# Optimization experiments

Measured on AMD Instinct MI355X. Metric: run time of the kernel, lower is better.

The kernel has to match this reference:

```python
import jax, jax.numpy as jnp
import numpy as np
from jax import lax

BEAM = 4
MAXLEN = 12
V, E, H = 32000, 256, 512
S, B = 512, 8


def lstm_cell(x, h, c, Wih, Whh, bih, bhh):
    # torch gate order: input, forget, cell, output
    g = x @ Wih.T + h @ Whh.T + bih + bhh
    i, f, gg, o = jnp.split(g, 4, axis=-1)
    c2 = jax.nn.sigmoid(f) * c + jax.nn.sigmoid(i) * jnp.tanh(gg)
    return jax.nn.sigmoid(o) * jnp.tanh(c2), c2


def lstm_layer(xs, Wih, Whh, bih, bhh):
    Bn, Hn = xs.shape[1], Whh.shape[1]
    h0 = jnp.zeros((Bn, Hn), xs.dtype)

    def step(carry, x):
        h, c = carry
        h, c = lstm_cell(x, h, c, Wih, Whh, bih, bhh)
        return (h, c), h

    (hT, cT), hs = lax.scan(step, (h0, h0), xs)
    return hs, hT, cT


def setup_inputs():
    key = jax.random.key(0)
    ks = jax.random.split(key, 32)

    def p(i, shape, s=0.08):
        return jax.random.normal(ks[i], shape, jnp.float32) * s

    return {
        'text': jax.random.randint(ks[0], (S, B), 0, V),
        'emb_enc': p(1, (V, E)),
        'emb_dec': p(2, (V, E)),
        'enc_Wih0': p(3, (4 * H, E)), 'enc_Whh0': p(4, (4 * H, H)),
        'enc_bih0': p(5, (4 * H,)), 'enc_bhh0': p(6, (4 * H,)),
        'enc_Wih1': p(7, (4 * H, H)), 'enc_Whh1': p(8, (4 * H, H)),
        'enc_bih1': p(9, (4 * H,)), 'enc_bhh1': p(10, (4 * H,)),
        'dec_Wih': p(11, (4 * H, E)), 'dec_Whh': p(12, (4 * H, H)),
        'dec_bih': p(13, (4 * H,)), 'dec_bhh': p(14, (4 * H,)),
        'Wq': p(15, (H, H)), 'bq': p(16, (H,)),
        'Wk': p(17, (H, H)), 'bk': p(18, (H,)),
        'Wv': p(19, (H, H)), 'bv': p(20, (H,)),
        'Wo': p(21, (H, H)), 'bo': p(22, (H,)),
        'Wout': p(23, (V, H)), 'bout': p(24, (V,)),
    }


def reference(text, emb_enc, emb_dec, enc_Wih0, enc_Whh0, enc_bih0, enc_bhh0,
              enc_Wih1, enc_Whh1, enc_bih1, enc_bhh1,
              dec_Wih, dec_Whh, dec_bih, dec_bhh,
              Wq, bq, Wk, bk, Wv, bv, Wo, bo, Wout, bout):
    # ---- encoder: 2-layer LSTM over source ----
    emb = emb_enc[text]                                   # [S, B, E]
    hs0, h0, c0 = lstm_layer(emb, enc_Wih0, enc_Whh0, enc_bih0, enc_bhh0)
    hs1, h1, c1 = lstm_layer(hs0, enc_Wih1, enc_Whh1, enc_bih1, enc_bhh1)
    enc_hidden = jnp.stack([h0, h1])                      # [L, B, H] final hidden per layer
    k_enc = enc_hidden @ Wk.T + bk                        # precompute encoder K/V projections
    v_enc = enc_hidden @ Wv.T + bv
    scale = 1.0 / jnp.sqrt(jnp.float32(H))

    # ---- beam state: all beams start from last encoder layer state ----
    dec_h = jnp.tile(h1[None], (BEAM, 1, 1))              # [BEAM, B, H]
    dec_c = jnp.tile(c1[None], (BEAM, 1, 1))
    T = MAXLEN + 1
    result = jnp.full((BEAM, T, B), 1, dtype=jnp.int32)   # SOS token = 1
    logits_hist = jnp.zeros((BEAM, T, B, V), jnp.float32).at[:, 0, :, 1].set(1.0)

    def step(carry, t):
        dh, dc, res, lh = carry
        tok = lax.dynamic_slice(res, (0, t, 0), (BEAM, 1, B))[:, 0, :]      # last token [BEAM, B]
        x = emb_dec[tok]                                                    # [BEAM, B, E]
        nh, nc = lstm_cell(x, dh, dc, dec_Wih, dec_Whh, dec_bih, dec_bhh)   # batched over beams
        # single-head attention: query = dec hidden, keys/values = [enc layers ; dec hidden]
        q = nh @ Wq.T + bq
        kd = nh @ Wk.T + bk
        vd = nh @ Wv.T + bv
        keys = jnp.concatenate([jnp.broadcast_to(k_enc[None], (BEAM,) + k_enc.shape), kd[:, None]], axis=1)  # [BEAM, L+1, B, H]
        vals = jnp.concatenate([jnp.broadcast_to(v_enc[None], (BEAM,) + v_enc.shape), vd[:, None]], axis=1)
        scores = jnp.einsum('nbh,nlbh->nbl', q, keys) * scale
        w = jax.nn.softmax(scores, axis=-1)
        ctx = jnp.einsum('nbl,nlbh->nbh', w, vals)
        dec_out = (ctx @ Wo.T + bo) @ Wout.T + bout                          # [BEAM, B, V]
        # per-beam top-k over vocab, then top-k over the BEAM*BEAM candidates
        pv, pt = lax.top_k(dec_out, BEAM)                                    # [BEAM, B, K]
        cand_v = jnp.transpose(pv, (1, 0, 2)).reshape(B, BEAM * BEAM)        # beam-major blocks
        cand_t = jnp.transpose(pt, (1, 0, 2)).reshape(B, BEAM * BEAM)
        _, ti = lax.top_k(cand_v, BEAM)                                      # [B, K]
        old_beam = (ti // BEAM).T                                            # [BEAM, B]
        new_tok = jnp.take_along_axis(cand_t, ti, axis=1).T                  # [BEAM, B]
        # vectorized beam reorder (gather) of state + history
        nh = jnp.take_along_axis(nh, old_beam[:, :, None], axis=0)
        nc = jnp.take_along_axis(nc, old_beam[:, :, None], axis=0)
        res = jnp.take_along_axis(res, old_beam[:, None, :], axis=0)
        lh = jnp.take_along_axis(lh, old_beam[:, None, :, None], axis=0)
        step_log = jnp.take_along_axis(dec_out, old_beam[:, :, None], axis=0)
        res = lax.dynamic_update_slice(res, new_tok[:, None, :].astype(jnp.int32), (0, t + 1, 0))
        lh = lax.dynamic_update_slice(lh, step_log[:, None], (0, t + 1, 0, 0))
        return (nh, nc, res, lh), None

    (dec_h, dec_c, result, logits_hist), _ = lax.scan(
        step, (dec_h, dec_c, result, logits_hist), jnp.arange(MAXLEN))
    output_res = result[0].T                               # [B, T]
    output_logits = jnp.transpose(logits_hist[0], (1, 2, 0))  # [B, V, T]
    return output_res, output_logits
```

## Files before the change

### kernel.cpp

```cpp
#include <hip/hip_runtime.h>
#include <hip/hip_bf16.h>
#include <float.h>


using ull = unsigned long long;

#define SCOPE_AGENT __HIP_MEMORY_SCOPE_AGENT

__device__ __forceinline__ float cLoad(const float* p) {
  return __hip_atomic_load(p, __ATOMIC_RELAXED, SCOPE_AGENT);
}
__device__ __forceinline__ void cStore(float* p, float v) {
  __hip_atomic_store(p, v, __ATOMIC_RELAXED, SCOPE_AGENT);
}
__device__ __forceinline__ int cLoadI(const int* p) {
  return __hip_atomic_load(p, __ATOMIC_RELAXED, SCOPE_AGENT);
}
__device__ __forceinline__ void cStoreI(int* p, int v) {
  __hip_atomic_store(p, v, __ATOMIC_RELAXED, SCOPE_AGENT);
}
__device__ __forceinline__ ull cLoad64(const ull* p) {
  return __hip_atomic_load(p, __ATOMIC_RELAXED, SCOPE_AGENT);
}
__device__ __forceinline__ void cStore64(ull* p, ull v) {
  __hip_atomic_store(p, v, __ATOMIC_RELAXED, SCOPE_AGENT);
}

__device__ __forceinline__ float2 u2f2(ull u) {
  union { ull u; float2 f; } c; c.u = u; return c.f;
}

__device__ __forceinline__ bool isSent(ull v) {
  return (unsigned)v == 0xFFFFFFFFu || (unsigned)(v >> 32) == 0xFFFFFFFFu;
}

__device__ __forceinline__ void fbar1(int* fl, int phase) {
  __syncthreads();
  if (threadIdx.x < 32)
    cStoreI(fl + (blockIdx.x * 32 + threadIdx.x) * 32, phase);
  {
    const int* f = fl + (threadIdx.x * 32 + (blockIdx.x >> 3)) * 32;
    while (cLoadI(f) < phase) {}
  }
  __syncthreads();
}

__device__ __forceinline__ float sig_(float x) { return 1.0f / (1.0f + expf(-x)); }

__device__ __forceinline__ void ins4(float* v, int* id, float nv, int ni) {
  if (nv > v[3] || (nv == v[3] && ni < id[3])) {
    v[3] = nv; id[3] = ni;
#pragma unroll
    for (int p = 3; p > 0; --p) {
      bool sw = (v[p] > v[p - 1]) || (v[p] == v[p - 1] && id[p] < id[p - 1]);
      if (sw) {
        float t0 = v[p]; v[p] = v[p - 1]; v[p - 1] = t0;
        int t1 = id[p]; id[p] = id[p - 1]; id[p - 1] = t1;
      }
    }
  }
}

struct EncP {
  const int* text; const float* emb;
  const float* Wih0; const float* Whh0; const float* bih0; const float* bhh0;
  const float* Wih1; const float* Whh1; const float* bih1; const float* bhh1;
  float* h0hist; float* h1hist;
  float* h0f; float* h1f; float* c1f;
};

template <int KX>
__device__ void enc_run(const EncP& P, float* xcat, int w, int tid) {
  constexpr int KTOT = KX + 512;
  constexpr int ST = KTOT + 4;
  constexpr int KSL = KTOT / 8;
  constexpr int Q = KSL / 4;
  constexpr int L = (KX == 512) ? 1 : 0;
  __shared__ float part[16 * 8 * 8];
  __shared__ float gl[128];

  const int c0 = (w & 127) * 4;
  const int kh = tid >> 5, col = (tid >> 3) & 3, b = tid & 7;
  const int kbase = kh * KSL;

  const float* Wih = L ? P.Wih1 : P.Wih0;
  const float* Whh = L ? P.Whh1 : P.Whh0;
  const float4* wih4[4]; const float4* whh4[4];
#pragma unroll
  for (int g = 0; g < 4; ++g) {
    const int row = g * 512 + c0 + col;
    wih4[g] = (const float4*)(Wih + (size_t)row * KX);
    whh4[g] = (const float4*)(Whh + (size_t)row * 512);
  }
  float bsum = 0.f;
  if (tid < 128) {
    const int r = tid >> 3;
    const int row = (r & 3) * 512 + c0 + (r >> 2);
    bsum = (L ? P.bih1[row] + P.bhh1[row] : P.bih0[row] + P.bhh0[row]);
  }
  float creg = 0.f;
  float* myHist = L ? P.h1hist : P.h0hist;

  int qx = (KX - kbase) / 4;
  qx = qx < 0 ? 0 : (qx > Q ? Q : qx);

  for (int e = tid; e < 4096; e += 256)
    xcat[(e >> 9) * ST + KX + (e & 511)] = 0.f;
  __syncthreads();

  for (int t = 0; t < 512; ++t) {
    if constexpr (KX == 256) {
      for (int e = tid; e < 1024; e += 256) {
        const int b2 = e >> 7, k2 = e & 127;
        const int tokv = P.text[t * 8 + b2];
        *(float2*)(xcat + b2 * ST + 2 * k2) =
            *(const float2*)(P.emb + (size_t)tokv * 256 + 2 * k2);
      }
      if (t >= 1) {
        const ull* hq = (const ull*)(myHist + (size_t)t * 4096) + tid;
        ull v[8];
#pragma unroll
        for (int z = 0; z < 8; ++z) v[z] = cLoad64(hq + z * 256);
        for (;;) {
          bool any = false;
#pragma unroll
          for (int z = 0; z < 8; ++z)
            if (isSent(v[z])) { v[z] = cLoad64(hq + z * 256); any = true; }
          if (!any) break;
        }
#pragma unroll
        for (int z = 0; z < 8; ++z)
          *(ull*)(xcat + z * ST + KX + 2 * tid) = v[z];
      }
    } else {
      const ull* xq0 = (const ull*)(P.h0hist + (size_t)(t + 1) * 4096) + tid;
      const ull* hq = (const ull*)(P.h1hist + (size_t)t * 4096) + tid;
      ull vx[8], vh[8];
#pragma unroll
      for (int z = 0; z < 8; ++z) vx[z] = cLoad64(xq0 + z * 256);
      if (t >= 1) {
#pragma unroll
        for (int z = 0; z < 8; ++z) vh[z] = cLoad64(hq + z * 256);
      }
      for (;;) {
        bool any = false;
#pragma unroll
        for (int z = 0; z < 8; ++z)
          if (isSent(vx[z])) { vx[z] = cLoad64(xq0 + z * 256); any = true; }
        if (t >= 1) {
#pragma unroll
          for (int z = 0; z < 8; ++z)
            if (isSent(vh[z])) { vh[z] = cLoad64(hq + z * 256); any = true; }
        }
        if (!any) break;
      }
#pragma unroll
      for (int z = 0; z < 8; ++z)
        *(ull*)(xcat + z * ST + 2 * tid) = vx[z];
      if (t >= 1) {
#pragma unroll
        for (int z = 0; z < 8; ++z)
          *(ull*)(xcat + z * ST + KX + 2 * tid) = vh[z];
      }
    }
    __syncthreads();

    float a0 = 0.f, a1 = 0.f, a2 = 0.f, a3 = 0.f;
    {
      const float4* xq = (const float4*)(xcat + b * ST + kbase);
      const int iw = kbase >> 2, ih = (kbase - KX) >> 2;
#pragma unroll 4
      for (int q = 0; q < qx; ++q) {
        float4 x = xq[q];
        float4 w0 = wih4[0][iw + q], w1 = wih4[1][iw + q];
        float4 w2 = wih4[2][iw + q], w3 = wih4[3][iw + q];
        a0 = fmaf(w0.x, x.x, a0); a0 = fmaf(w0.y, x.y, a0);
        a0 = fmaf(w0.z, x.z, a0); a0 = fmaf(w0.w, x.w, a0);
        a1 = fmaf(w1.x, x.x, a1); a1 = fmaf(w1.y, x.y, a1);
        a1 = fmaf(w1.z, x.z, a1); a1 = fmaf(w1.w, x.w, a1);
        a2 = fmaf(w2.x, x.x, a2); a2 = fmaf(w2.y, x.y, a2);
        a2 = fmaf(w2.z, x.z, a2); a2 = fmaf(w2.w, x.w, a2);
        a3 = fmaf(w3.x, x.x, a3); a3 = fmaf(w3.y, x.y, a3);
        a3 = fmaf(w3.z, x.z, a3); a3 = fmaf(w3.w, x.w, a3);
      }
#pragma unroll 4
      for (int q = qx; q < Q; ++q) {
        float4 x = xq[q];
        float4 w0 = whh4[0][ih + q], w1 = whh4[1][ih + q];
        float4 w2 = whh4[2][ih + q], w3 = whh4[3][ih + q];
        a0 = fmaf(w0.x, x.x, a0); a0 = fmaf(w0.y, x.y, a0);
        a0 = fmaf(w0.z, x.z, a0); a0 = fmaf(w0.w, x.w, a0);
        a1 = fmaf(w1.x, x.x, a1); a1 = fmaf(w1.y, x.y, a1);
        a1 = fmaf(w1.z, x.z, a1); a1 = fmaf(w1.w, x.w, a1);
        a2 = fmaf(w2.x, x.x, a2); a2 = fmaf(w2.y, x.y, a2);
        a2 = fmaf(w2.z, x.z, a2); a2 = fmaf(w2.w, x.w, a2);
        a3 = fmaf(w3.x, x.x, a3); a3 = fmaf(w3.y, x.y, a3);
        a3 = fmaf(w3.z, x.z, a3); a3 = fmaf(w3.w, x.w, a3);
      }
    }
    part[((col * 4 + 0) * 8 + b) * 8 + kh] = a0;
    part[((col * 4 + 1) * 8 + b) * 8 + kh] = a1;
    part[((col * 4 + 2) * 8 + b) * 8 + kh] = a2;
    part[((col * 4 + 3) * 8 + b) * 8 + kh] = a3;
    __syncthreads();
    if (tid < 128) {
      const int r = tid >> 3, b2 = tid & 7;
      const float4* pp = (const float4*)(part + (r * 8 + b2) * 8);
      float4 p0 = pp[0], p1 = pp[1];
      gl[r * 8 + b2] =
          bsum + (((p0.x + p0.y) + (p0.z + p0.w)) + ((p1.x + p1.y) + (p1.z + p1.w)));
    }
    __syncthreads();
    if (tid < 32) {
      const int cc = tid >> 3, b2 = tid & 7;
      float gi = gl[(cc * 4 + 0) * 8 + b2], gf_ = gl[(cc * 4 + 1) * 8 + b2];
      float gg = gl[(cc * 4 + 2) * 8 + b2], go = gl[(cc * 4 + 3) * 8 + b2];
      float c2 = sig_(gf_) * creg + sig_(gi) * tanhf(gg);
      float hv = sig_(go) * tanhf(c2);
      creg = c2;
      cStore(myHist + (size_t)(t + 1) * 4096 + b2 * 512 + c0 + cc, hv);
      if (t == 511) {
        (L ? P.h1f : P.h0f)[b2 * 512 + c0 + cc] = hv;
        if (L) P.c1f[b2 * 512 + c0 + cc] = c2;
      }
    }
    __syncthreads();
  }
}

__global__ __launch_bounds__(256, 1) void enc_kernel(EncP P) {
  __shared__ float xcat0[8 * 772];
  __shared__ float xcat1[8 * 1028];
  if (blockIdx.x >> 7) enc_run<512>(P, xcat1, blockIdx.x, threadIdx.x);
  else enc_run<256>(P, xcat0, blockIdx.x, threadIdx.x);
}

__global__ __launch_bounds__(256) void prep_kernel(
    const float* Wk, const float* bk, const float* Wv, const float* bv,
    const float* h0f, const float* h1f, const float* c1f,
    float* kenc, float* venc, float* nhb, float* ncb) {
  const int w = blockIdx.x, tid = threadIdx.x;
  if (w < 64) {
    const int o = w * 256 + tid;
    const int kv = o >> 13, l = (o >> 12) & 1, b = (o >> 9) & 7, c = o & 511;
    const float4* h4 = (const float4*)((l ? h1f : h0f) + b * 512);
    const float4* w4 = (const float4*)((kv ? Wv : Wk) + (size_t)c * 512);
    float s0 = 0.f, s1 = 0.f, s2 = 0.f, s3 = 0.f;
#pragma unroll 8
    for (int k = 0; k < 128; ++k) {
      float4 a = w4[k], x = h4[k];
      s0 = fmaf(a.x, x.x, s0); s1 = fmaf(a.y, x.y, s1);
      s2 = fmaf(a.z, x.z, s2); s3 = fmaf(a.w, x.w, s3);
    }
    (kv ? venc : kenc)[l * 4096 + b * 512 + c] =
        (kv ? bv : bk)[c] + ((s0 + s1) + (s2 + s3));
  } else {
    const int o = (w - 64) * 256 + tid;
    nhb[16384 + o] = h1f[o & 4095];
    ncb[16384 + o] = c1f[o & 4095];
  }
}

__global__ __launch_bounds__(256) void prep2_kernel(
    const float* Wq, const float* Wk, const float* Wv, const float* Wo,
    const float* bq, const float* bk, const float* bv,
    const float* kenc, const float* venc,
    float* At, float* W2, float* u, float* pvec, float* veWo, float* bvo,
    float* sl0, float* sbb) {
  const int w = blockIdx.x, tid = threadIdx.x;
#pragma unroll 1
  for (int sub = 0; sub < 2; ++sub) {
    const int d = 2 * w + sub;
    for (int cc = 0; cc < 2; ++cc) {
      const int c = tid + cc * 256;
      float s0 = 0.f, s1 = 0.f, s2 = 0.f, s3 = 0.f;
      for (int i = 0; i < 512; i += 4) {
        s0 = fmaf(Wk[(i + 0) * 512 + d], Wq[(i + 0) * 512 + c], s0);
        s1 = fmaf(Wk[(i + 1) * 512 + d], Wq[(i + 1) * 512 + c], s1);
        s2 = fmaf(Wk[(i + 2) * 512 + d], Wq[(i + 2) * 512 + c], s2);
        s3 = fmaf(Wk[(i + 3) * 512 + d], Wq[(i + 3) * 512 + c], s3);
      }
      At[(size_t)d * 512 + c] = (s0 + s1) + (s2 + s3);
    }
    for (int cc = 0; cc < 2; ++cc) {
      const int dc = tid + cc * 256;
      float s0 = 0.f, s1 = 0.f, s2 = 0.f, s3 = 0.f;
      const float* wor = Wo + (size_t)d * 512;
      for (int c2 = 0; c2 < 512; c2 += 4) {
        s0 = fmaf(wor[c2 + 0], Wv[(size_t)(c2 + 0) * 512 + dc], s0);
        s1 = fmaf(wor[c2 + 1], Wv[(size_t)(c2 + 1) * 512 + dc], s1);
        s2 = fmaf(wor[c2 + 2], Wv[(size_t)(c2 + 2) * 512 + dc], s2);
        s3 = fmaf(wor[c2 + 3], Wv[(size_t)(c2 + 3) * 512 + dc], s3);
      }
      W2[(size_t)d * 512 + dc] = (s0 + s1) + (s2 + s3);
    }
  }
  if (w == 0) {
    for (int cc = 0; cc < 2; ++cc) {
      const int c = tid + cc * 256;
      float a = 0.f;
      for (int i = 0; i < 512; ++i)
        a += Wq[i * 512 + c] * bk[i] + Wk[i * 512 + c] * bq[i];
      u[c] = a;
    }
  } else if (w <= 32) {
    const int idx = (w - 1) * 256 + tid;
    const int l = idx >> 12, b = (idx >> 9) & 7, c = idx & 511;
    const float* ke = kenc + l * 4096 + b * 512;
    float a = 0.f;
    for (int i = 0; i < 512; ++i) a = fmaf(Wq[i * 512 + c], ke[i], a);
    pvec[idx] = a;
  } else if (w <= 64) {
    const int idx = (w - 33) * 256 + tid;
    const int l = idx >> 12, b = (idx >> 9) & 7, j = idx & 511;
    const float* ve = venc + l * 4096 + b * 512;
    const float* wo = Wo + (size_t)j * 512;
    float a = 0.f;
    for (int c = 0; c < 512; ++c) a = fmaf(wo[c], ve[c], a);
    veWo[idx] = a;
  } else if (w == 65) {
    for (int cc = 0; cc < 2; ++cc) {
      const int j = tid + cc * 256;
      const float* wo = Wo + (size_t)j * 512;
      float a = 0.f;
      for (int c = 0; c < 512; ++c) a = fmaf(wo[c], bv[c], a);
      bvo[j] = a;
    }
  } else if (w == 66) {
    if (tid < 16) {
      const int l = tid >> 3, b = tid & 7;
      const float* ke = kenc + l * 4096 + b * 512;
      float a = 0.f;
      for (int i = 0; i < 512; ++i) a = fmaf(bq[i], ke[i], a);
      sl0[tid] = a;
    } else if (tid == 16) {
      float a = 0.f;
      for (int i = 0; i < 512; ++i) a = fmaf(bq[i], bk[i], a);
      sbb[0] = a;
    }
  }
}

__global__ __launch_bounds__(256) void prep3_kernel(
    const float* Wout, const float* bout, const float* bo, const float* veWo,
    float* E0g, float* E1g, float* bcg) {
  __shared__ float sv[16 * 516 + 512];
  __shared__ float stg[8 * 516];
  const int w = blockIdx.x, tid = threadIdx.x;
  for (int e = tid; e < 8704; e += 256) {
    if (e < 8192) sv[(e >> 9) * 516 + (e & 511)] = veWo[e];
    else sv[16 * 516 + (e - 8192)] = bo[e - 8192];
  }
  const int cbase = w * 125;
  for (int tile = 0; tile < 16; ++tile) {
    const int r0 = tile * 8;
    __syncthreads();
    for (int e = tid; e < 1024; e += 256) {
      const int rr = e >> 7, k4 = e & 127;
      int row = r0 + rr; if (row > 124) row = 124;
      *(float4*)&stg[rr * 516 + k4 * 4] =
          *(const float4*)&Wout[(size_t)(cbase + row) * 512 + k4 * 4];
    }
    __syncthreads();
    if (tid < 136) {
      const int rr = tid / 17, sel = tid - rr * 17;
      const int row = r0 + rr;
      if (row < 125) {
        const float4* a4 = (const float4*)&stg[rr * 516];
        const float4* x4 =
            (const float4*)&sv[sel < 16 ? sel * 516 : 16 * 516];
        float s0 = 0.f, s1 = 0.f, s2 = 0.f, s3 = 0.f;
#pragma unroll 8
        for (int k = 0; k < 128; ++k) {
          float4 a = a4[k], x = x4[k];
          s0 = fmaf(a.x, x.x, s0); s1 = fmaf(a.y, x.y, s1);
          s2 = fmaf(a.z, x.z, s2); s3 = fmaf(a.w, x.w, s3);
        }
        const float s = (s0 + s1) + (s2 + s3);
        const int c = cbase + row;
        if (sel < 16) (sel < 8 ? E0g : E1g)[(size_t)(sel & 7) * 32000 + c] = s;
        else bcg[c] = s + bout[c];
      }
    }
  }
}

struct DecP {
  const float* emb;
  const float* Wih; const float* Whh; const float* bih; const float* bhh;
  const float* Wout;
  const float* At; const float* W2; const float* u; const float* bvo;
  const float* pvec; const float* sl0; const float* sbb;
  const float* E0g; const float* E1g; const float* bcg;
  float* nhb; float* ncb;
  float* vbuf;
  float* part_s;
  ull* pvp;
  int* obh;
  int* res0;
  __hip_bfloat16* hist;
  int* fl;
};

__global__ __launch_bounds__(256, 1) void dec_kernel(DecP P) {
  __shared__ float SM[29600];
  __shared__ float gl[2][4][32];
  __shared__ float slS[32][3];
  __shared__ float wslS[96];
  __shared__ float svv[32][8][4];
  __shared__ int sii[32][8][4];
  __shared__ float rvS[32][4];
  __shared__ int rtS[32][4];
  __shared__ int resS[4][13][8];
  __shared__ int oblS[32];
  __shared__ int tokS[32];
  __shared__ float pscS[32][8];
  __shared__ float nhsS[32][8];

  const int w = blockIdx.x, tid = threadIdx.x;
  float* hs = SM;
  float* tileS = SM;
  float* vqS = SM + 16896;
  float* tvE = SM + 21120;
  int* tiE = (int*)(SM + 25344);
  int ph = 0;

  if (tid < 104) {
    for (int n = 0; n < 4; ++n) resS[n][tid >> 3][tid & 7] = 1;
  }

  auto do_select = [&](int tt) {
    {
      const int r = tid >> 3, ch = tid & 7;
      float m4[4] = {-FLT_MAX, -FLT_MAX, -FLT_MAX, -FLT_MAX};
      int mi[4] = {0x7fffffff, 0x7fffffff, 0x7fffffff, 0x7fffffff};
      for (int g = 0; g < 4; ++g) {
        ull pk[32];
#pragma unroll
        for (int z = 0; z < 32; ++z) {
          const int wg = ch * 32 + g * 8 + (z >> 2);
          pk[z] = cLoad64(P.pvp + wg * 128 + r * 4 + (z & 3));
        }
#pragma unroll
        for (int z = 0; z < 32; ++z)
          ins4(m4, mi, __uint_as_float((unsigned)(pk[z] >> 32)),
               (int)(unsigned)(pk[z] & 0xffffffffu));
      }
#pragma unroll
      for (int k = 0; k < 4; ++k) { svv[r][ch][k] = m4[k]; sii[r][ch][k] = mi[k]; }
    }
    __syncthreads();
    if (tid < 32) {
      float m4[4] = {-FLT_MAX, -FLT_MAX, -FLT_MAX, -FLT_MAX};
      int mi[4] = {0x7fffffff, 0x7fffffff, 0x7fffffff, 0x7fffffff};
      for (int g2 = 0; g2 < 8; ++g2)
#pragma unroll
        for (int k = 0; k < 4; ++k) ins4(m4, mi, svv[tid][g2][k], sii[tid][g2][k]);
#pragma unroll
      for (int k = 0; k < 4; ++k) { rvS[tid][k] = m4[k]; rtS[tid][k] = mi[k]; }
    }
    __syncthreads();
    if (tid < 8) {
      const int b2 = tid;
      unsigned used = 0;
      int obl_[4], tkl_[4];
#pragma unroll
      for (int sel = 0; sel < 4; ++sel) {
        float bestv = -FLT_MAX; int bestj = -1;
        for (int j = 0; j < 16; ++j) {
          if (used & (1u << j)) continue;
          float vv = rvS[(j >> 2) * 8 + b2][j & 3];
          if (vv > bestv) { bestv = vv; bestj = j; }
        }
        used |= 1u << bestj;
        const int obn = bestj >> 2;
        obl_[sel] = obn;
        tkl_[sel] = rtS[obn * 8 + b2][bestj & 3];
        oblS[sel * 8 + b2] = obn;
        tokS[sel * 8 + b2] = tkl_[sel];
        if (w == 0) P.obh[tt * 32 + sel * 8 + b2] = obn;
      }
      if (w == 0) {
        int tmp[4][13];
        for (int n2 = 0; n2 < 4; ++n2)
          for (int s2 = 0; s2 < 13; ++s2) tmp[n2][s2] = resS[obl_[n2]][s2][b2];
        for (int n2 = 0; n2 < 4; ++n2)
          for (int s2 = 0; s2 < 13; ++s2) resS[n2][s2][b2] = tmp[n2][s2];
        for (int n2 = 0; n2 < 4; ++n2) resS[n2][tt + 1][b2] = tkl_[n2];
      }
    }
    __syncthreads();
    if (tt == 11 && w == 0 && tid < 104)
      P.res0[tid] = resS[0][tid >> 3][tid & 7];
  };

  for (int t = 0; t < 12; ++t) {
    const int curOff = (t & 1) * 16384, prevOff = ((t + 1) & 1) * 16384;

    if (t == 0) {
      __syncthreads();
      if (tid < 32) { oblS[tid] = tid >> 3; tokS[tid] = 1; }
      __syncthreads();
    } else {
      do_select(t - 1);
    }
    {
      const int col_l = tid >> 7, gate = (tid >> 5) & 3, nb = tid & 31;
      const int col = 2 * w + col_l;
      const int row = gate * 512 + col;
      for (int e = tid; e < 2048; e += 256) {
        const int nb2 = e >> 6, kf = e & 63;
        float4 v = *((const float4*)(P.emb + (size_t)tokS[nb2] * 256) + kf);
        *((float4*)hs + nb2 * 65 + kf) = v;
      }
      __syncthreads();
      float s0 = 0.f, s1 = 0.f, s2 = 0.f, s3 = 0.f;
      {
        const float4* a4 = (const float4*)(P.Wih + (size_t)row * 256);
        const float4* x4 = (const float4*)hs + nb * 65;
#pragma unroll 8
        for (int k = 0; k < 64; ++k) {
          float4 a = a4[k], x = x4[k];
          s0 = fmaf(a.x, x.x, s0); s1 = fmaf(a.y, x.y, s1);
          s2 = fmaf(a.z, x.z, s2); s3 = fmaf(a.w, x.w, s3);
        }
      }
      float acc = P.bih[row] + P.bhh[row];
      const ull* hsrc = (const ull*)(P.nhb + prevOff);
      const float4* w4row = (const float4*)(P.Whh + (size_t)row * 512);
      for (int ck = 0; ck < 2; ++ck) {
        __syncthreads();
        for (int e = tid; e < 4096; e += 256) {
          const int nb2 = e >> 7, k2 = e & 127;
          const int srow = oblS[nb2] * 8 + (nb2 & 7);
          ull v = cLoad64(hsrc + srow * 256 + ck * 128 + k2);
          *(ull*)(hs + nb2 * 260 + 2 * k2) = v;
        }
        __syncthreads();
        const float4* h4 = (const float4*)hs + nb * 65;
        const float4* w4 = w4row + ck * 64;
#pragma unroll 8
        for (int k = 0; k < 64; ++k) {
          float4 a = w4[k], x = h4[k];
          s0 = fmaf(a.x, x.x, s0); s1 = fmaf(a.y, x.y, s1);
          s2 = fmaf(a.z, x.z, s2); s3 = fmaf(a.w, x.w, s3);
        }
      }
      acc += (s0 + s1) + (s2 + s3);
      gl[col_l][gate][nb] = acc;
      __syncthreads();
      if (tid < 64) {
        const int cc = tid >> 5, nb2 = tid & 31;
        const int col2 = 2 * w + cc;
        float gi = gl[cc][0][nb2], gf_ = gl[cc][1][nb2];
        float gg = gl[cc][2][nb2], go = gl[cc][3][nb2];
        const int srow = oblS[nb2] * 8 + (nb2 & 7);
        float cold = cLoad(P.ncb + prevOff + srow * 512 + col2);
        float c2 = sig_(gf_) * cold + sig_(gi) * tanhf(gg);
        float hv = sig_(go) * tanhf(c2);
        cStore(P.nhb + curOff + nb2 * 512 + col2, hv);
        cStore(P.ncb + curOff + nb2 * 512 + col2, c2);
      }
    }
    fbar1(P.fl, ++ph);

    if (w < 128) {
      const int p = w >> 6, cb = w & 63;
      const int col_l = tid >> 5, nb = tid & 31;
      const int col = cb * 8 + col_l;
      const float* W = (p ? P.W2 : P.At) + (size_t)col * 512;
      float acc = (p ? P.bvo : P.u)[col];
      {
        const float4* w4row = (const float4*)W;
        float s0 = 0.f, s1 = 0.f, s2 = 0.f, s3 = 0.f;
        for (int ck = 0; ck < 2; ++ck) {
          __syncthreads();
          const ull* s8 = (const ull*)(P.nhb + curOff);
          for (int e = tid; e < 4096; e += 256) {
            const int nb2 = e >> 7, k2 = e & 127;
            ull v = cLoad64(s8 + nb2 * 256 + ck * 128 + k2);
            *(ull*)(hs + nb2 * 260 + 2 * k2) = v;
          }
          __syncthreads();
          const float4* h4 = (const float4*)hs + nb * 65;
          const float4* w4 = w4row + ck * 64;
#pragma unroll 8
          for (int k = 0; k < 64; ++k) {
            float4 a = w4[k], x = h4[k];
            s0 = fmaf(a.x, x.x, s0); s1 = fmaf(a.y, x.y, s1);
            s2 = fmaf(a.z, x.z, s2); s3 = fmaf(a.w, x.w, s3);
          }
        }
        acc += (s0 + s1) + (s2 + s3);
      }
      if (p) {
        cStore(P.vbuf + nb * 512 + col, acc);
      } else {
        const float nhv = cLoad(P.nhb + curOff + nb * 512 + col);
        pscS[nb][col_l] = nhv * acc;
        nhsS[nb][col_l] = nhv;
        __syncthreads();
        if (tid < 32) {
          const int nb2 = tid, b = nb2 & 7;
          float s2a = 0.f, l0 = 0.f, l1 = 0.f;
#pragma unroll
          for (int i2 = 0; i2 < 8; ++i2) {
            s2a += pscS[nb2][i2];
            const float nv = nhsS[nb2][i2];
            l0 = fmaf(nv, P.pvec[b * 512 + cb * 8 + i2], l0);
            l1 = fmaf(nv, P.pvec[4096 + b * 512 + cb * 8 + i2], l1);
          }
          cStore(P.part_s + (0 * 32 + nb2) * 64 + cb, l0);
          cStore(P.part_s + (1 * 32 + nb2) * 64 + cb, l1);
          cStore(P.part_s + (2 * 32 + nb2) * 64 + cb, s2a);
        }
      }
    }
    fbar1(P.fl, ++ph);

    {
      const int cbase = w * 125;
      if (tid < 96) {
        const int nb = tid / 3, l = tid - (tid / 3) * 3, b = nb & 7;
        const ull* ps = (const ull*)(P.part_s + (l * 32 + nb) * 64);
        ull pk[32];
#pragma unroll
        for (int z = 0; z < 32; ++z) pk[z] = cLoad64(ps + z);
        float s = 0.f;
#pragma unroll
        for (int z = 0; z < 32; ++z) { float2 f = u2f2(pk[z]); s += f.x + f.y; }
        const float bias = (l < 2) ? P.sl0[l * 8 + b] : P.sbb[0];
        slS[nb][l] = (s + bias) * (1.0f / sqrtf(512.0f));
      }
      __syncthreads();
      if (tid < 32) {
        float a = slS[tid][0], b2 = slS[tid][1], c3 = slS[tid][2];
        float m = fmaxf(a, fmaxf(b2, c3));
        float e0 = expf(a - m), e1 = expf(b2 - m), e2 = expf(c3 - m);
        float inv = 1.0f / (e0 + e1 + e2);
        wslS[tid * 3 + 0] = e0 * inv;
        wslS[tid * 3 + 1] = e1 * inv;
        wslS[tid * 3 + 2] = e2 * inv;
      }
      const int rg = tid >> 3, ng = tid & 7;
      float acc[4][4];
#pragma unroll
      for (int i = 0; i < 4; ++i)
#pragma unroll
        for (int j = 0; j < 4; ++j) acc[i][j] = 0.f;
      for (int q = 0; q < 4; ++q) {
        __syncthreads();
        for (int e = tid; e < 1024; e += 256) {
          const int nb = e >> 5, kf = e & 31;
          ull u0 = cLoad64((const ull*)(P.vbuf + nb * 512 + q * 128 + kf * 4));
          ull u1 = cLoad64((const ull*)(P.vbuf + nb * 512 + q * 128 + kf * 4 + 2));
          float2 a = u2f2(u0), b2 = u2f2(u1);
          float4 v = {a.x, a.y, b2.x, b2.y};
          *(float4*)(vqS + (nb & 3) * 1056 + (nb >> 2) * 132 + kf * 4) = v;
        }
        for (int it = 0; it < 16; ++it) {
          const int idx = it * 256 + tid;
          if (idx < 4000) {
            const int r = idx >> 5, kf = idx & 31;
            float4 v = *(const float4*)(P.Wout + (size_t)(cbase + r) * 512 +
                                        q * 128 + kf * 4);
            *(float4*)(tileS + (r & 3) * 4224 + (r >> 2) * 132 + kf * 4) = v;
          }
        }
        __syncthreads();
        for (int kf = 0; kf < 32; ++kf) {
          float4 xv[4], wv[4];
#pragma unroll
          for (int j = 0; j < 4; ++j)
            xv[j] = *(const float4*)(vqS + j * 1056 + ng * 132 + kf * 4);
#pragma unroll
          for (int i = 0; i < 4; ++i)
            wv[i] = *(const float4*)(tileS + i * 4224 + rg * 132 + kf * 4);
#pragma unroll
          for (int i = 0; i < 4; ++i)
#pragma unroll
            for (int j = 0; j < 4; ++j) {
              float a = acc[i][j];
              a = fmaf(wv[i].x, xv[j].x, a); a = fmaf(wv[i].y, xv[j].y, a);
              a = fmaf(wv[i].z, xv[j].z, a); a = fmaf(wv[i].w, xv[j].w, a);
              acc[i][j] = a;
            }
        }
      }
      __syncthreads();
      float w0w[4], w1w[4], w2w[4];
#pragma unroll
      for (int j = 0; j < 4; ++j) {
        const int nb = ng * 4 + j;
        w0w[j] = wslS[nb * 3 + 0]; w1w[j] = wslS[nb * 3 + 1]; w2w[j] = wslS[nb * 3 + 2];
      }
      float v4[4][4]; int i4[4][4];
#pragma unroll
      for (int j = 0; j < 4; ++j)
#pragma unroll
        for (int k = 0; k < 4; ++k) { v4[j][k] = -FLT_MAX; i4[j][k] = 0x7fffffff; }
#pragma unroll
      for (int i = 0; i < 4; ++i) {
        const int r = rg * 4 + i;
        if (r < 125) {
          const int c = cbase + r;
          const float bcv = P.bcg[c];
#pragma unroll
          for (int j = 0; j < 4; ++j) {
            const int nb = ng * 4 + j, b = nb & 7;
            const float e0 = P.E0g[(size_t)b * 32000 + c];
            const float e1 = P.E1g[(size_t)b * 32000 + c];
            const float L = fmaf(w2w[j], acc[i][j],
                                 fmaf(w0w[j], e0, fmaf(w1w[j], e1, bcv)));
            P.hist[(size_t)t * 1024000 + (size_t)nb * 32000 + c] = __float2bfloat16(L);
            ins4(v4[j], i4[j], L, c);
          }
        }
      }
#pragma unroll
      for (int j = 0; j < 4; ++j)
#pragma unroll
        for (int k = 0; k < 4; ++k) {
          tvE[(ng * 4 + j) * 132 + rg * 4 + k] = v4[j][k];
          tiE[(ng * 4 + j) * 132 + rg * 4 + k] = i4[j][k];
        }
      __syncthreads();
      if (tid < 32) {
        float m4[4] = {-FLT_MAX, -FLT_MAX, -FLT_MAX, -FLT_MAX};
        int mi[4] = {0x7fffffff, 0x7fffffff, 0x7fffffff, 0x7fffffff};
        for (int e = 0; e < 128; ++e)
          ins4(m4, mi, tvE[tid * 132 + e], tiE[tid * 132 + e]);
#pragma unroll
        for (int k = 0; k < 4; ++k) {
          ull pk = ((ull)__float_as_uint(m4[k]) << 32) | (unsigned)mi[k];
          cStore64(P.pvp + w * 128 + tid * 4 + k, pk);
        }
      }
    }
    fbar1(P.fl, ++ph);
  }
  if (w == 0) do_select(11);
}

__global__ __launch_bounds__(256) void out_kernel(const __hip_bfloat16* hist,
                                                  const int* obh, const int* res0,
                                                  float* out) {
  __shared__ float sh[13 * 1000];
  __shared__ int sbArr[12];
  const int w = blockIdx.x, tid = threadIdx.x;
  const int b = w >> 5, v0 = (w & 31) * 1000;
  if (tid == 0) {
    int beta = 0;
    for (int t = 11; t >= 0; --t) {
      const int sb = obh[t * 32 + beta * 8 + b];
      sbArr[t] = sb;
      beta = sb;
    }
  }
  __syncthreads();
  for (int e = tid; e < 12000; e += 256) {
    const int t = e / 1000, vv = e - t * 1000;
    sh[(t + 1) * 1000 + vv] = __bfloat162float(
        hist[(size_t)(t * 32 + sbArr[t] * 8 + b) * 32000 + v0 + vv]);
  }
  for (int e = tid; e < 1000; e += 256) sh[e] = (v0 + e == 1) ? 1.0f : 0.0f;
  __syncthreads();
  float* base = out + 104 + (size_t)(b * 32000 + v0) * 13;
  for (int o = tid; o < 13000; o += 256) {
    const int v = o / 13, t = o - v * 13;
    base[o] = sh[t * 1000 + v];
  }
  if (w == 0 && tid < 104) {
    out[(tid & 7) * 13 + (tid >> 3)] = (float)res0[tid];
  }
}

extern "C" void kernel_launch(void* const* d_in, const int* in_sizes, int n_in,
                              void* d_out, int out_size, void* d_ws, size_t ws_size,
                              hipStream_t stream) {
  const int* text  = (const int*)d_in[0];
  const float* embE = (const float*)d_in[1];
  const float* embD = (const float*)d_in[2];
  const float* Wih0 = (const float*)d_in[3];
  const float* Whh0 = (const float*)d_in[4];
  const float* bih0 = (const float*)d_in[5];
  const float* bhh0 = (const float*)d_in[6];
  const float* Wih1 = (const float*)d_in[7];
  const float* Whh1 = (const float*)d_in[8];
  const float* bih1 = (const float*)d_in[9];
  const float* bhh1 = (const float*)d_in[10];
  const float* dWih = (const float*)d_in[11];
  const float* dWhh = (const float*)d_in[12];
  const float* dbih = (const float*)d_in[13];
  const float* dbhh = (const float*)d_in[14];
  const float* Wq = (const float*)d_in[15];
  const float* bq = (const float*)d_in[16];
  const float* Wk = (const float*)d_in[17];
  const float* bk = (const float*)d_in[18];
  const float* Wv = (const float*)d_in[19];
  const float* bv = (const float*)d_in[20];
  const float* Wo = (const float*)d_in[21];
  const float* bo = (const float*)d_in[22];
  const float* Wout = (const float*)d_in[23];
  const float* bout = (const float*)d_in[24];

  char* ws = (char*)d_ws;
  size_t off = 0;
  auto alloc = [&](size_t bytes) -> char* {
    off = (off + 511) & ~(size_t)511;
    char* p = ws + off;
    off += bytes;
    return p;
  };
  float* h0hist = (float*)alloc((size_t)513 * 4096 * 4);
  float* h1hist = (float*)alloc((size_t)513 * 4096 * 4);
  int* decFl  = (int*)alloc((size_t)262144 * 4);
  float* h0f  = (float*)alloc(4096 * 4);
  float* h1f  = (float*)alloc(4096 * 4);
  float* c1f  = (float*)alloc(4096 * 4);
  float* kenc = (float*)alloc(8192 * 4);
  float* venc = (float*)alloc(8192 * 4);
  float* At   = (float*)alloc((size_t)262144 * 4);
  float* W2   = (float*)alloc((size_t)262144 * 4);
  float* u    = (float*)alloc(512 * 4);
  float* pvec = (float*)alloc(8192 * 4);
  float* veWo = (float*)alloc(8192 * 4);
  float* bvo  = (float*)alloc(512 * 4);
  float* sl0  = (float*)alloc(16 * 4);
  float* sbb  = (float*)alloc(32 * 4);
  float* E0g  = (float*)alloc((size_t)256000 * 4);
  float* E1g  = (float*)alloc((size_t)256000 * 4);
  float* bcg  = (float*)alloc(32000 * 4);
  float* nhb  = (float*)alloc(2 * 16384 * 4);
  float* ncb  = (float*)alloc(2 * 16384 * 4);
  float* vbuf = (float*)alloc(16384 * 4);
  float* part_s = (float*)alloc(6144 * 4);
  ull* pvp    = (ull*)alloc((size_t)32768 * 8);
  int* obh    = (int*)alloc(384 * 4);
  int* res0   = (int*)alloc(104 * 4);
  __hip_bfloat16* hist = (__hip_bfloat16*)alloc((size_t)12288000 * 2);
  if (off > ws_size) return;

  hipMemsetAsync(h0hist, 0xFF, (size_t)513 * 4096 * 4, stream);
  hipMemsetAsync(h1hist, 0xFF, (size_t)513 * 4096 * 4, stream);
  hipMemsetAsync(decFl, 0, (size_t)262144 * 4, stream);

  EncP ep{text, embE, Wih0, Whh0, bih0, bhh0, Wih1, Whh1, bih1, bhh1,
          h0hist, h1hist, h0f, h1f, c1f};
  enc_kernel<<<256, 256, 0, stream>>>(ep);

  prep_kernel<<<128, 256, 0, stream>>>(Wk, bk, Wv, bv, h0f, h1f, c1f, kenc, venc,
                                       nhb, ncb);
  prep2_kernel<<<256, 256, 0, stream>>>(Wq, Wk, Wv, Wo, bq, bk, bv, kenc, venc,
                                        At, W2, u, pvec, veWo, bvo, sl0, sbb);
  prep3_kernel<<<256, 256, 0, stream>>>(Wout, bout, bo, veWo, E0g, E1g, bcg);

  DecP dp{embD, dWih, dWhh, dbih, dbhh, Wout,
          At, W2, u, bvo, pvec, sl0, sbb, E0g, E1g, bcg,
          nhb, ncb, vbuf, part_s, pvp, obh, res0, hist, decFl};
  dec_kernel<<<256, 256, 0, stream>>>(dp);

  out_kernel<<<256, 256, 0, stream>>>(hist, obh, res0, (float*)d_out);
}
```

Measured before the change: 6.337 ms.

## Overlap encoder-independent weight precomputation with the encoder kernel via extra blocks

Work that depends only on the weights (Wk^T·Wq, Wo·Wv, u, bvo, sbb, and the bo-projected output bias) moves out of the post-encoder prep kernels into 256 extra blocks appended to the encoder launch. The recurrent encoder blocks raise their wave priority with s_setprio so the added blocks use idle CUs without slowing the serial LSTM. This shortens the prep kernels that sit on the critical path after the encoder. The risk is that the wing blocks compete with the encoder for memory bandwidth or CU residency. If the encoder's cross-block synchronisation assumes all 256 LSTM blocks are co-resident, the extra blocks could also delay scheduling.

Result: faster. 5.812 ms (-8.3%).

```diff
diff --git a/kernel.cpp b/kernel.cpp
--- a/kernel.cpp
+++ b/kernel.cpp
@@ -67,6 +67,10 @@
   const float* Wih1; const float* Whh1; const float* bih1; const float* bhh1;
   float* h0hist; float* h1hist;
   float* h0f; float* h1f; float* c1f;
+  const float* Wq; const float* Wk; const float* Wv; const float* Wo;
+  const float* bq; const float* bk; const float* bv; const float* bo;
+  const float* Wout; const float* bout;
+  float* At; float* W2; float* u; float* bvo; float* sbb; float* bcg;
 };
 
 template <int KX>
@@ -228,9 +232,80 @@
   }
 }
 
+__device__ void enc_wing(const EncP& P, int wgw, int tid) {
+#pragma unroll 1
+  for (int sub = 0; sub < 2; ++sub) {
+    const int d = 2 * wgw + sub;
+    for (int cc = 0; cc < 2; ++cc) {
+      const int c = tid + cc * 256;
+      float s0 = 0.f, s1 = 0.f, s2 = 0.f, s3 = 0.f;
+      for (int i = 0; i < 512; i += 4) {
+        s0 = fmaf(P.Wk[(i + 0) * 512 + d], P.Wq[(i + 0) * 512 + c], s0);
+        s1 = fmaf(P.Wk[(i + 1) * 512 + d], P.Wq[(i + 1) * 512 + c], s1);
+        s2 = fmaf(P.Wk[(i + 2) * 512 + d], P.Wq[(i + 2) * 512 + c], s2);
+        s3 = fmaf(P.Wk[(i + 3) * 512 + d], P.Wq[(i + 3) * 512 + c], s3);
+      }
+      P.At[(size_t)d * 512 + c] = (s0 + s1) + (s2 + s3);
+    }
+    for (int cc = 0; cc < 2; ++cc) {
+      const int dc = tid + cc * 256;
+      float s0 = 0.f, s1 = 0.f, s2 = 0.f, s3 = 0.f;
+      const float* wor = P.Wo + (size_t)d * 512;
+      for (int c2 = 0; c2 < 512; c2 += 4) {
+        s0 = fmaf(wor[c2 + 0], P.Wv[(size_t)(c2 + 0) * 512 + dc], s0);
+        s1 = fmaf(wor[c2 + 1], P.Wv[(size_t)(c2 + 1) * 512 + dc], s1);
+        s2 = fmaf(wor[c2 + 2], P.Wv[(size_t)(c2 + 2) * 512 + dc], s2);
+        s3 = fmaf(wor[c2 + 3], P.Wv[(size_t)(c2 + 3) * 512 + dc], s3);
+      }
+      P.W2[(size_t)d * 512 + dc] = (s0 + s1) + (s2 + s3);
+    }
+  }
+  if (tid < 125) {
+    const int c = wgw * 125 + tid;
+    const float4* wr = (const float4*)(P.Wout + (size_t)c * 512);
+    const float4* bo4 = (const float4*)P.bo;
+    float s0 = 0.f, s1 = 0.f, s2 = 0.f, s3 = 0.f;
+#pragma unroll 8
+    for (int k = 0; k < 128; ++k) {
+      float4 a = wr[k], x = bo4[k];
+      s0 = fmaf(a.x, x.x, s0); s1 = fmaf(a.y, x.y, s1);
+      s2 = fmaf(a.z, x.z, s2); s3 = fmaf(a.w, x.w, s3);
+    }
+    P.bcg[c] = (s0 + s1) + (s2 + s3) + P.bout[c];
+  }
+  if (wgw == 0) {
+    for (int cc = 0; cc < 2; ++cc) {
+      const int c = tid + cc * 256;
+      float a = 0.f;
+      for (int i = 0; i < 512; ++i)
+        a += P.Wq[i * 512 + c] * P.bk[i] + P.Wk[i * 512 + c] * P.bq[i];
+      P.u[c] = a;
+    }
+  } else if (wgw == 65) {
+    for (int cc = 0; cc < 2; ++cc) {
+      const int j = tid + cc * 256;
+      const float* wo = P.Wo + (size_t)j * 512;
+      float a = 0.f;
+      for (int c = 0; c < 512; ++c) a = fmaf(wo[c], P.bv[c], a);
+      P.bvo[j] = a;
+    }
+  } else if (wgw == 66) {
+    if (tid == 0) {
+      float a = 0.f;
+      for (int i = 0; i < 512; ++i) a = fmaf(P.bq[i], P.bk[i], a);
+      P.sbb[0] = a;
+    }
+  }
+}
+
 __global__ __launch_bounds__(256, 1) void enc_kernel(EncP P) {
   __shared__ float xcat0[8 * 772];
   __shared__ float xcat1[8 * 1028];
+  if (blockIdx.x >= 256) {
+    enc_wing(P, blockIdx.x - 256, threadIdx.x);
+    return;
+  }
+  __builtin_amdgcn_s_setprio(1);
   if (blockIdx.x >> 7) enc_run<512>(P, xcat1, blockIdx.x, threadIdx.x);
   else enc_run<256>(P, xcat0, blockIdx.x, threadIdx.x);
 }
@@ -261,96 +336,44 @@
   }
 }
 
-__global__ __launch_bounds__(256) void prep2_kernel(
-    const float* Wq, const float* Wk, const float* Wv, const float* Wo,
-    const float* bq, const float* bk, const float* bv,
+__global__ __launch_bounds__(256) void prep2b_kernel(
+    const float* Wq, const float* Wo, const float* bq,
     const float* kenc, const float* venc,
-    float* At, float* W2, float* u, float* pvec, float* veWo, float* bvo,
-    float* sl0, float* sbb) {
+    float* pvec, float* veWo, float* sl0) {
   const int w = blockIdx.x, tid = threadIdx.x;
-#pragma unroll 1
-  for (int sub = 0; sub < 2; ++sub) {
-    const int d = 2 * w + sub;
-    for (int cc = 0; cc < 2; ++cc) {
-      const int c = tid + cc * 256;
-      float s0 = 0.f, s1 = 0.f, s2 = 0.f, s3 = 0.f;
-      for (int i = 0; i < 512; i += 4) {
-        s0 = fmaf(Wk[(i + 0) * 512 + d], Wq[(i + 0) * 512 + c], s0);
-        s1 = fmaf(Wk[(i + 1) * 512 + d], Wq[(i + 1) * 512 + c], s1);
-        s2 = fmaf(Wk[(i + 2) * 512 + d], Wq[(i + 2) * 512 + c], s2);
-        s3 = fmaf(Wk[(i + 3) * 512 + d], Wq[(i + 3) * 512 + c], s3);
-      }
-      At[(size_t)d * 512 + c] = (s0 + s1) + (s2 + s3);
-    }
-    for (int cc = 0; cc < 2; ++cc) {
-      const int dc = tid + cc * 256;
-      float s0 = 0.f, s1 = 0.f, s2 = 0.f, s3 = 0.f;
-      const float* wor = Wo + (size_t)d * 512;
-      for (int c2 = 0; c2 < 512; c2 += 4) {
-        s0 = fmaf(wor[c2 + 0], Wv[(size_t)(c2 + 0) * 512 + dc], s0);
-        s1 = fmaf(wor[c2 + 1], Wv[(size_t)(c2 + 1) * 512 + dc], s1);
-        s2 = fmaf(wor[c2 + 2], Wv[(size_t)(c2 + 2) * 512 + dc], s2);
-        s3 = fmaf(wor[c2 + 3], Wv[(size_t)(c2 + 3) * 512 + dc], s3);
-      }
-      W2[(size_t)d * 512 + dc] = (s0 + s1) + (s2 + s3);
-    }
-  }
-  if (w == 0) {
-    for (int cc = 0; cc < 2; ++cc) {
-      const int c = tid + cc * 256;
-      float a = 0.f;
-      for (int i = 0; i < 512; ++i)
-        a += Wq[i * 512 + c] * bk[i] + Wk[i * 512 + c] * bq[i];
-      u[c] = a;
-    }
-  } else if (w <= 32) {
-    const int idx = (w - 1) * 256 + tid;
+  if (w < 32) {
+    const int idx = w * 256 + tid;
     const int l = idx >> 12, b = (idx >> 9) & 7, c = idx & 511;
     const float* ke = kenc + l * 4096 + b * 512;
     float a = 0.f;
     for (int i = 0; i < 512; ++i) a = fmaf(Wq[i * 512 + c], ke[i], a);
     pvec[idx] = a;
-  } else if (w <= 64) {
-    const int idx = (w - 33) * 256 + tid;
+  } else if (w < 64) {
+    const int idx = (w - 32) * 256 + tid;
     const int l = idx >> 12, b = (idx >> 9) & 7, j = idx & 511;
     const float* ve = venc + l * 4096 + b * 512;
     const float* wo = Wo + (size_t)j * 512;
     float a = 0.f;
     for (int c = 0; c < 512; ++c) a = fmaf(wo[c], ve[c], a);
     veWo[idx] = a;
-  } else if (w == 65) {
-    for (int cc = 0; cc < 2; ++cc) {
-      const int j = tid + cc * 256;
-      const float* wo = Wo + (size_t)j * 512;
-      float a = 0.f;
-      for (int c = 0; c < 512; ++c) a = fmaf(wo[c], bv[c], a);
-      bvo[j] = a;
-    }
-  } else if (w == 66) {
+  } else {
     if (tid < 16) {
       const int l = tid >> 3, b = tid & 7;
       const float* ke = kenc + l * 4096 + b * 512;
       float a = 0.f;
       for (int i = 0; i < 512; ++i) a = fmaf(bq[i], ke[i], a);
       sl0[tid] = a;
-    } else if (tid == 16) {
-      float a = 0.f;
-      for (int i = 0; i < 512; ++i) a = fmaf(bq[i], bk[i], a);
-      sbb[0] = a;
     }
   }
 }
 
 __global__ __launch_bounds__(256) void prep3_kernel(
-    const float* Wout, const float* bout, const float* bo, const float* veWo,
-    float* E0g, float* E1g, float* bcg) {
-  __shared__ float sv[16 * 516 + 512];
+    const float* Wout, const float* veWo, float* E0g, float* E1g) {
+  __shared__ float sv[16 * 516];
   __shared__ float stg[8 * 516];
   const int w = blockIdx.x, tid = threadIdx.x;
-  for (int e = tid; e < 8704; e += 256) {
-    if (e < 8192) sv[(e >> 9) * 516 + (e & 511)] = veWo[e];
-    else sv[16 * 516 + (e - 8192)] = bo[e - 8192];
-  }
+  for (int e = tid; e < 8192; e += 256)
+    sv[(e >> 9) * 516 + (e & 511)] = veWo[e];
   const int cbase = w * 125;
   for (int tile = 0; tile < 16; ++tile) {
     const int r0 = tile * 8;
@@ -362,13 +385,12 @@
           *(const float4*)&Wout[(size_t)(cbase + row) * 512 + k4 * 4];
     }
     __syncthreads();
-    if (tid < 136) {
-      const int rr = tid / 17, sel = tid - rr * 17;
+    if (tid < 128) {
+      const int rr = tid >> 4, sel = tid & 15;
       const int row = r0 + rr;
       if (row < 125) {
         const float4* a4 = (const float4*)&stg[rr * 516];
-        const float4* x4 =
-            (const float4*)&sv[sel < 16 ? sel * 516 : 16 * 516];
+        const float4* x4 = (const float4*)&sv[sel * 516];
         float s0 = 0.f, s1 = 0.f, s2 = 0.f, s3 = 0.f;
 #pragma unroll 8
         for (int k = 0; k < 128; ++k) {
@@ -377,9 +399,7 @@
           s2 = fmaf(a.z, x.z, s2); s3 = fmaf(a.w, x.w, s3);
         }
         const float s = (s0 + s1) + (s2 + s3);
-        const int c = cbase + row;
-        if (sel < 16) (sel < 8 ? E0g : E1g)[(size_t)(sel & 7) * 32000 + c] = s;
-        else bcg[c] = s + bout[c];
+        (sel < 8 ? E0g : E1g)[(size_t)(sel & 7) * 32000 + cbase + row] = s;
       }
     }
   }
@@ -846,14 +866,15 @@
   hipMemsetAsync(decFl, 0, (size_t)262144 * 4, stream);
 
   EncP ep{text, embE, Wih0, Whh0, bih0, bhh0, Wih1, Whh1, bih1, bhh1,
-          h0hist, h1hist, h0f, h1f, c1f};
-  enc_kernel<<<256, 256, 0, stream>>>(ep);
+          h0hist, h1hist, h0f, h1f, c1f,
+          Wq, Wk, Wv, Wo, bq, bk, bv, bo, Wout, bout,
+          At, W2, u, bvo, sbb, bcg};
+  enc_kernel<<<512, 256, 0, stream>>>(ep);
 
   prep_kernel<<<128, 256, 0, stream>>>(Wk, bk, Wv, bv, h0f, h1f, c1f, kenc, venc,
                                        nhb, ncb);
-  prep2_kernel<<<256, 256, 0, stream>>>(Wq, Wk, Wv, Wo, bq, bk, bv, kenc, venc,
-                                        At, W2, u, pvec, veWo, bvo, sl0, sbb);
-  prep3_kernel<<<256, 256, 0, stream>>>(Wout, bout, bo, veWo, E0g, E1g, bcg);
+  prep2b_kernel<<<65, 256, 0, stream>>>(Wq, Wo, bq, kenc, venc, pvec, veWo, sl0);
+  prep3_kernel<<<256, 256, 0, stream>>>(Wout, veWo, E0g, E1g);
 
   DecP dp{embD, dWih, dWhh, dbih, dbhh, Wout,
           At, W2, u, bvo, pvec, sl0, sbb, E0g, E1g, bcg,
```
